# Kernel optimization log

Hardware: AMD Instinct MI355X
Metric: run time of the kernel (lower is better)

The kernel has to match this reference:

```python
import jax, jax.numpy as jnp
import numpy as np

E = 1024      # embed_dim
QH = 16       # query heads
KVH = 4       # kv heads
HD = E // QH  # head_dim = 64
KVE = HD * KVH  # 256
EPS = 1e-5
ROPE_BASE = 10000.0


def rope(x, d):
    # Faithful to the source RoPE: d == number of heads (x.shape[-2]),
    # and the 'sequence' axis of the cache is x.shape[0] (the batch dim).
    # rope(x) = x*cos + (x*sin) * neg_half(x)  (note: nonlinear in x).
    b = x.shape[0]
    theta = 1.0 / (ROPE_BASE ** (jnp.arange(0, d, 2, dtype=jnp.float32) / d))  # (d//2,)
    seq_idx = jnp.arange(b, dtype=jnp.float32)                                 # (b,)
    idx_theta = seq_idx[:, None] * theta[None, :]                              # (b, d//2)
    idx2 = jnp.concatenate([idx_theta, idx_theta], axis=-1)                    # (b, d)
    # cached shape (b,1,1,d); source permutes (0,1,3,2) -> (b,1,d,1)
    cos = jnp.cos(idx2)[:, None, :, None]  # (b,1,d,1)
    sin = jnp.sin(idx2)[:, None, :, None]
    d2 = d // 2
    # split of the LAST dim (head_dim) at d//2 == num_heads//2, as in source
    neg = jnp.concatenate([-x[..., d2:], x[..., :d2]], axis=-1)
    return x * cos + (x * sin) * neg


def setup_inputs() -> dict:
    key = jax.random.key(0)
    ks = jax.random.split(key, 12)
    b, n = 1, 2048

    def xavier(k, shape):
        fan_out, fan_in = shape
        std = (2.0 / (fan_in + fan_out)) ** 0.5
        return jax.random.normal(k, shape, dtype=jnp.float32) * std

    return {
        "query": jax.random.normal(ks[0], (b, n, E), dtype=jnp.float32),
        "key": jax.random.normal(ks[1], (b, n, E), dtype=jnp.float32),
        "value": jax.random.normal(ks[2], (b, n, E), dtype=jnp.float32),
        "Wq": xavier(ks[3], (E, E)),
        "bq": jnp.zeros((E,), jnp.float32),
        "Wk": xavier(ks[4], (KVE, E)),
        "bk": jnp.zeros((KVE,), jnp.float32),
        "Wv": xavier(ks[5], (KVE, E)),
        "bv": jnp.zeros((KVE,), jnp.float32),
        "gamma": jnp.ones((E,), jnp.float32),
        "beta": jnp.zeros((E,), jnp.float32),
    }


def reference(query, key, value, Wq, bq, Wk, bk, Wv, bv, gamma, beta):
    b, n, _ = query.shape
    q = query @ Wq.T + bq            # (b,n,E)
    k = key @ Wk.T + bk              # (b,n,KVE)
    v = value @ Wv.T + bv            # (b,n,KVE)

    q = q.reshape(b, n, QH, HD)      # b n h d
    k = k.reshape(b, n, KVH, HD)
    v = v.reshape(b, n, KVH, HD)

    q = rope(q, QH)
    k = rope(k, KVH)

    # b n h d -> b h n d
    q = jnp.transpose(q, (0, 2, 1, 3))
    k = jnp.transpose(k, (0, 2, 1, 3))
    v = jnp.transpose(v, (0, 2, 1, 3))

    scale = float(HD) ** 0.5
    q = q / scale

    g = QH // KVH
    # 'b (h g) n d -> b g h n d' : h outer, g inner
    q = q.reshape(b, KVH, g, n, HD)              # (b, h, g, n, d)
    q = jnp.transpose(q, (0, 2, 1, 3, 4))        # (b, g, h, n, d)

    sim = jnp.einsum('bghnd,bhsd->bghns', q, k)  # (b,g,h,n,s)
    attn = jax.nn.softmax(sim, axis=-1)
    out = jnp.einsum('bghns,bhsd->bghnd', attn, v)

    # 'b g h n d -> b n (h g) d'
    out = jnp.transpose(out, (0, 3, 2, 1, 4))    # (b, n, h, g, d)
    x = out.reshape(b, n, QH * HD)               # (b, n, E)

    # LayerNorm (biased variance, as in torch)
    mu = jnp.mean(x, axis=-1, keepdims=True)
    var = jnp.mean((x - mu) ** 2, axis=-1, keepdims=True)
    x = (x - mu) * jax.lax.rsqrt(var + EPS) * gamma + beta

    # NOTE: source computes out_proj(x) but returns x, so out_proj is dead code.
    return x
```

## Files before the change

### kernel.cpp

```cpp
#include <hip/hip_runtime.h>
#include <math.h>

#define EDIM   1024
#define KVEDIM 256
#define HDIM   64
#define QHEADS 16

typedef __attribute__((ext_vector_type(8))) short short8;
typedef __attribute__((ext_vector_type(4))) float f32x4;

__device__ __forceinline__ unsigned pack2(float a, float b) {
    unsigned ua = __builtin_bit_cast(unsigned, a);
    unsigned ub = __builtin_bit_cast(unsigned, b);
    ua += 0x7fffu + ((ua >> 16) & 1u);
    ub += 0x7fffu + ((ub >> 16) & 1u);
    return (ua >> 16) | (ub & 0xffff0000u);
}
__device__ __forceinline__ short f2b(float a) {
    unsigned ua = __builtin_bit_cast(unsigned, a);
    ua += 0x7fffu + ((ua >> 16) & 1u);
    return (short)(ua >> 16);
}
__device__ __forceinline__ unsigned cvtpk(float a, float b) {
    unsigned r;
    asm("v_cvt_pk_bf16_f32 %0, %1, %2" : "=v"(r) : "v"(a), "v"(b));
    return r;
}

__global__ __launch_bounds__(256)
void cvt_bf16(const float* __restrict__ s0, const float* __restrict__ s1,
              const float* __restrict__ s2, const float* __restrict__ s3,
              const float* __restrict__ s4, const float* __restrict__ s5,
              short* __restrict__ d0, short* __restrict__ d1,
              short* __restrict__ d2, short* __restrict__ d3,
              short* __restrict__ d4, short* __restrict__ d5,
              int n0, int n1, int n2, int n3, int n4, int n5)
{
    const float* s; short* d; int n;
    switch (blockIdx.y) {
        case 0: s = s0; d = d0; n = n0; break;
        case 1: s = s1; d = d1; n = n1; break;
        case 2: s = s2; d = d2; n = n2; break;
        case 3: s = s3; d = d3; n = n3; break;
        case 4: s = s4; d = d4; n = n4; break;
        default: s = s5; d = d5; n = n5; break;
    }
    int i = ((int)blockIdx.x * 256 + threadIdx.x) * 8;
    if (i >= n) return;
    float4 a = *(const float4*)&s[i];
    float4 b = *(const float4*)&s[i + 4];
    uint4 o;
    o.x = pack2(a.x, a.y); o.y = pack2(a.z, a.w);
    o.z = pack2(b.x, b.y); o.w = pack2(b.z, b.w);
    *(uint4*)&d[i] = o;
}

__global__ __launch_bounds__(256)
void proj_gemm(const short* __restrict__ Aq, const short* __restrict__ Ak,
               const short* __restrict__ Av,
               const short* __restrict__ Wqb, const short* __restrict__ Wkb,
               const short* __restrict__ Wvb,
               const float* __restrict__ bq, const float* __restrict__ bk,
               const float* __restrict__ bv,
               short* __restrict__ Cq, short* __restrict__ Ck,
               short* __restrict__ Cv, float qscale)
{
    const int bid = blockIdx.x;
    const short* A; const short* W; const float* bias; short* C;
    int N, bm, bn; float scale;
    if (bid < 128) {
        A = Aq; W = Wqb; bias = bq; C = Cq; N = EDIM; scale = qscale;
        bm = (bid >> 3) * 128; bn = (bid & 7) * 128;
    } else if (bid < 160) {
        int i = bid - 128;
        A = Ak; W = Wkb; bias = bk; C = Ck; N = KVEDIM; scale = 1.0f;
        bm = (i >> 1) * 128; bn = (i & 1) * 128;
    } else {
        int i = bid - 160;
        A = Av; W = Wvb; bias = bv; C = Cv; N = KVEDIM; scale = 1.0f;
        bm = (i >> 1) * 128; bn = (i & 1) * 128;
    }
    const int K = EDIM;

    __shared__ short As[128 * 72];
    __shared__ short Ws[128 * 72];

    const int t = threadIdx.x, lane = t & 63, wv = t >> 6;
    const int lm = lane & 15, quad = lane >> 4;
    const int q8 = quad * 8, q4 = quad * 4;
    const int wm = (wv & 1) * 64, wn = (wv >> 1) * 64;
    const int sr = t >> 3, sc = (t & 7) * 8;

    f32x4 zero = {0.f, 0.f, 0.f, 0.f};
    f32x4 acc[4][4];
    #pragma unroll
    for (int i = 0; i < 4; ++i)
        #pragma unroll
        for (int j = 0; j < 4; ++j) acc[i][j] = zero;

    for (int k0 = 0; k0 < K; k0 += 64) {
        __syncthreads();
        #pragma unroll
        for (int i = 0; i < 4; ++i) {
            int r = sr + i * 32;
            *(uint4*)&As[r * 72 + sc] = *(const uint4*)&A[(size_t)(bm + r) * K + k0 + sc];
            *(uint4*)&Ws[r * 72 + sc] = *(const uint4*)&W[(size_t)(bn + r) * K + k0 + sc];
        }
        __syncthreads();
        #pragma unroll
        for (int ks = 0; ks < 2; ++ks) {
            short8 af[4], bfr[4];
            #pragma unroll
            for (int i = 0; i < 4; ++i)
                af[i] = *(const short8*)&As[(wm + i * 16 + lm) * 72 + ks * 32 + q8];
            #pragma unroll
            for (int j = 0; j < 4; ++j)
                bfr[j] = *(const short8*)&Ws[(wn + j * 16 + lm) * 72 + ks * 32 + q8];
            #pragma unroll
            for (int i = 0; i < 4; ++i)
                #pragma unroll
                for (int j = 0; j < 4; ++j)
                    acc[i][j] = __builtin_amdgcn_mfma_f32_16x16x32_bf16(
                        af[i], bfr[j], acc[i][j], 0, 0, 0);
        }
    }

    #pragma unroll
    for (int j = 0; j < 4; ++j) {
        float bj = bias[bn + wn + j * 16 + lm];
        #pragma unroll
        for (int i = 0; i < 4; ++i)
            #pragma unroll
            for (int r = 0; r < 4; ++r)
                C[(size_t)(bm + wm + i * 16 + q4 + r) * N + bn + wn + j * 16 + lm] =
                    f2b((acc[i][j][r] + bj) * scale);
    }
}

__global__ __launch_bounds__(256)
void attn_mfma(const short* __restrict__ q, const short* __restrict__ k,
               const short* __restrict__ v, float* __restrict__ x,
               float* __restrict__ opart, float* __restrict__ lpart,
               int n, int s_len, int partial)
{
    __shared__ short Ks[64 * 72];
    __shared__ short Vt[64 * 72];
    __shared__ short Ps[64 * 72];
    __shared__ float Lred[4][64];

    const int qh = blockIdx.y, kvh = qh >> 2;
    const int r0 = blockIdx.x * 64;
    const int t = threadIdx.x;
    const int lane = t & 63, wv = t >> 6;
    const int lm = lane & 15, quad = lane >> 4;
    const int q8 = quad * 8, q4 = quad * 4;

    short8 qf[4][2];
    #pragma unroll
    for (int qt = 0; qt < 4; ++qt) {
        const short* qrow = &q[(size_t)(r0 + qt * 16 + lm) * EDIM + qh * HDIM];
        qf[qt][0] = *(const short8*)&qrow[q8];
        qf[qt][1] = *(const short8*)&qrow[32 + q8];
    }

    const int rt0 = (wv & 1) * 2;
    const int dt0 = (wv >> 1) * 2;

    f32x4 zero = {0.f, 0.f, 0.f, 0.f};
    f32x4 oacc[2][2];
    #pragma unroll
    for (int i = 0; i < 2; ++i)
        #pragma unroll
        for (int j = 0; j < 2; ++j) oacc[i][j] = zero;
    float lp[4] = {0.f, 0.f, 0.f, 0.f};

    const int krow = t >> 2, kc = (t & 3) * 8;
    const int vs4 = (t & 15) * 4, vd0 = (t >> 4) * 4;

    const int s_lo = (int)blockIdx.z * s_len;
    for (int s0 = s_lo; s0 < s_lo + s_len; s0 += 64) {
        __syncthreads();
        {
            const uint4* ksrc = (const uint4*)&k[(size_t)(s0 + krow) * KVEDIM + kvh * HDIM];
            uint4 ka = ksrc[t & 3];
            uint4 kb = ksrc[(t & 3) + 4];
            *(uint4*)&Ks[krow * 72 + kc] = ka;
            *(uint4*)&Ks[krow * 72 + kc + 32] = kb;
        }
        {
            unsigned vr[4][2];
            #pragma unroll
            for (int i = 0; i < 4; ++i) {
                uint2 vv = *(const uint2*)&v[(size_t)(s0 + vs4 + i) * KVEDIM + kvh * HDIM + vd0];
                vr[i][0] = vv.x; vr[i][1] = vv.y;
            }
            #pragma unroll
            for (int j = 0; j < 4; ++j) {
                const unsigned sel = (j & 1) ? 0x07060302u : 0x05040100u;
                const int w = j >> 1;
                uint2 o;
                o.x = __builtin_amdgcn_perm(vr[1][w], vr[0][w], sel);
                o.y = __builtin_amdgcn_perm(vr[3][w], vr[2][w], sel);
                *(uint2*)&Vt[(vd0 + j) * 72 + vs4] = o;
            }
        }
        __syncthreads();

        short8 kf0 = *(const short8*)&Ks[(wv * 16 + lm) * 72 + q8];
        short8 kf1 = *(const short8*)&Ks[(wv * 16 + lm) * 72 + 32 + q8];
        #pragma unroll
        for (int qt = 0; qt < 4; ++qt) {
            f32x4 s = zero;
            s = __builtin_amdgcn_mfma_f32_16x16x32_bf16(kf0, qf[qt][0], s, 0, 0, 0);
            s = __builtin_amdgcn_mfma_f32_16x16x32_bf16(kf1, qf[qt][1], s, 0, 0, 0);
            float p0 = exp2f(s[0]);
            float p1 = exp2f(s[1]);
            float p2 = exp2f(s[2]);
            float p3 = exp2f(s[3]);
            lp[qt] += (p0 + p1) + (p2 + p3);
            uint2 pw; pw.x = cvtpk(p0, p1); pw.y = cvtpk(p2, p3);
            *(uint2*)&Ps[(qt * 16 + lm) * 72 + wv * 16 + q4] = pw;
        }
        __syncthreads();

        short8 vf[2][2];
        #pragma unroll
        for (int j = 0; j < 2; ++j) {
            vf[j][0] = *(const short8*)&Vt[((dt0 + j) * 16 + lm) * 72 + q8];
            vf[j][1] = *(const short8*)&Vt[((dt0 + j) * 16 + lm) * 72 + 32 + q8];
        }
        #pragma unroll
        for (int i = 0; i < 2; ++i) {
            short8 pf0 = *(const short8*)&Ps[((rt0 + i) * 16 + lm) * 72 + q8];
            short8 pf1 = *(const short8*)&Ps[((rt0 + i) * 16 + lm) * 72 + 32 + q8];
            #pragma unroll
            for (int j = 0; j < 2; ++j) {
                oacc[i][j] = __builtin_amdgcn_mfma_f32_16x16x32_bf16(pf0, vf[j][0], oacc[i][j], 0, 0, 0);
                oacc[i][j] = __builtin_amdgcn_mfma_f32_16x16x32_bf16(pf1, vf[j][1], oacc[i][j], 0, 0, 0);
            }
        }
    }

    #pragma unroll
    for (int qt = 0; qt < 4; ++qt) {
        float l = lp[qt];
        l += __shfl_xor(l, 16);
        l += __shfl_xor(l, 32);
        if (lane < 16) Lred[wv][qt * 16 + lm] = l;
    }
    __syncthreads();

    if (partial) {
        float* xp = opart + (size_t)blockIdx.z * n * EDIM;
        #pragma unroll
        for (int i = 0; i < 2; ++i) {
            #pragma unroll
            for (int r = 0; r < 4; ++r) {
                int row = (rt0 + i) * 16 + q4 + r;
                float lsum = (Lred[0][row] + Lred[1][row]) + (Lred[2][row] + Lred[3][row]);
                if (dt0 == 0 && lm == 0)
                    lpart[(size_t)blockIdx.z * n * QHEADS + (size_t)(r0 + row) * QHEADS + qh] = lsum;
                #pragma unroll
                for (int j = 0; j < 2; ++j)
                    xp[(size_t)(r0 + row) * EDIM + qh * HDIM + (dt0 + j) * 16 + lm] =
                        oacc[i][j][r];
            }
        }
    } else {
        #pragma unroll
        for (int i = 0; i < 2; ++i) {
            #pragma unroll
            for (int r = 0; r < 4; ++r) {
                int row = (rt0 + i) * 16 + q4 + r;
                float lsum = (Lred[0][row] + Lred[1][row]) + (Lred[2][row] + Lred[3][row]);
                float inv = 1.0f / lsum;
                #pragma unroll
                for (int j = 0; j < 2; ++j)
                    x[(size_t)(r0 + row) * EDIM + qh * HDIM + (dt0 + j) * 16 + lm] =
                        oacc[i][j][r] * inv;
            }
        }
    }
}

__global__ __launch_bounds__(256)
void ln_kernel(float* __restrict__ x, const float* __restrict__ gamma,
               const float* __restrict__ beta,
               const float* __restrict__ opart, const float* __restrict__ lpart,
               int nsplit, int n)
{
    const int row = blockIdx.x;
    const int t = threadIdx.x;

    float4 xv;
    if (nsplit > 0) {
        const int head = t >> 4;
        float l = 0.f;
        float4 s = {0.f, 0.f, 0.f, 0.f};
        for (int z = 0; z < nsplit; ++z) {
            const float4 o = *(const float4*)&opart[(size_t)z * n * EDIM +
                                                    (size_t)row * EDIM + t * 4];
            s.x += o.x; s.y += o.y; s.z += o.z; s.w += o.w;
            l += lpart[(size_t)z * n * QHEADS + (size_t)row * QHEADS + head];
        }
        const float inv = 1.f / l;
        xv.x = s.x * inv; xv.y = s.y * inv; xv.z = s.z * inv; xv.w = s.w * inv;
    } else {
        xv = *(const float4*)&x[(size_t)row * EDIM + t * 4];
    }

    float sm  = xv.x + xv.y + xv.z + xv.w;
    float sq = xv.x * xv.x + xv.y * xv.y + xv.z * xv.z + xv.w * xv.w;
    #pragma unroll
    for (int m = 1; m < 64; m <<= 1) {
        sm += __shfl_xor(sm, m);
        sq += __shfl_xor(sq, m);
    }
    __shared__ float ws_[4], wq_[4];
    const int wave = t >> 6;
    if ((t & 63) == 0) { ws_[wave] = sm; wq_[wave] = sq; }
    __syncthreads();
    sm = ws_[0] + ws_[1] + ws_[2] + ws_[3];
    sq = wq_[0] + wq_[1] + wq_[2] + wq_[3];

    const float mu   = sm * (1.f / EDIM);
    const float var  = sq * (1.f / EDIM) - mu * mu;
    const float rstd = rsqrtf(var + 1e-5f);

    float4 g = *(const float4*)&gamma[t * 4];
    float4 b = *(const float4*)&beta[t * 4];
    float4 o;
    o.x = (xv.x - mu) * rstd * g.x + b.x;
    o.y = (xv.y - mu) * rstd * g.y + b.y;
    o.z = (xv.z - mu) * rstd * g.z + b.z;
    o.w = (xv.w - mu) * rstd * g.w + b.w;
    *(float4*)&x[(size_t)row * EDIM + t * 4] = o;
}

extern "C" void kernel_launch(void* const* d_in, const int* in_sizes, int n_in,
                              void* d_out, int out_size, void* d_ws, size_t ws_size,
                              hipStream_t stream)
{
    const float* query = (const float*)d_in[0];
    const float* key   = (const float*)d_in[1];
    const float* value = (const float*)d_in[2];
    const float* Wq    = (const float*)d_in[3];
    const float* bq    = (const float*)d_in[4];
    const float* Wk    = (const float*)d_in[5];
    const float* bk    = (const float*)d_in[6];
    const float* Wv    = (const float*)d_in[7];
    const float* bv    = (const float*)d_in[8];
    const float* gamma = (const float*)d_in[9];
    const float* beta  = (const float*)d_in[10];
    float* out = (float*)d_out;

    const int n = in_sizes[0] / EDIM;

    short* qa  = (short*)d_ws;
    short* ka  = qa  + (size_t)n * EDIM;
    short* va  = ka  + (size_t)n * EDIM;
    short* wqb = va  + (size_t)n * EDIM;
    short* wkb = wqb + (size_t)EDIM * EDIM;
    short* wvb = wkb + (size_t)KVEDIM * EDIM;
    short* qb  = wvb + (size_t)KVEDIM * EDIM;
    short* kb  = qb  + (size_t)n * EDIM;
    short* vb  = kb  + (size_t)n * KVEDIM;
    short* ws_end = vb + (size_t)n * KVEDIM;

    const size_t base_bytes = (size_t)((char*)ws_end - (char*)d_ws);
    int nsplit = 0;
    for (int cand = 4; cand >= 1; cand >>= 1) {
        if (n % (64 * cand)) continue;
        size_t need = base_bytes +
                      (size_t)cand * ((size_t)n * EDIM + (size_t)n * QHEADS) * sizeof(float);
        if (need <= ws_size) { nsplit = cand; break; }
    }
    float* opart = (float*)ws_end;
    float* lpart = opart + (size_t)(nsplit > 0 ? nsplit : 1) * n * EDIM;

    const float qscale = 0.125f * 1.44269504088896f;

    cvt_bf16<<<dim3(1024, 6), 256, 0, stream>>>(
        query, key, value, Wq, Wk, Wv,
        qa, ka, va, wqb, wkb, wvb,
        n * EDIM, n * EDIM, n * EDIM, EDIM * EDIM, KVEDIM * EDIM, KVEDIM * EDIM);

    proj_gemm<<<dim3(192), 256, 0, stream>>>(
        qa, ka, va, wqb, wkb, wvb, bq, bk, bv, qb, kb, vb, qscale);

    const int zdim  = (nsplit > 0) ? nsplit : 1;
    const int s_len = n / zdim;
    attn_mfma<<<dim3(n / 64, QHEADS, zdim), 256, 0, stream>>>(
        qb, kb, vb, out, opart, lpart, n, s_len, nsplit > 0 ? 1 : 0);

    ln_kernel<<<dim3(n), 256, 0, stream>>>(out, gamma, beta, opart, lpart, nsplit, n);
}
```

Measured before the change: 173.4 us.

## Restructure attention: one block per KV head, four query heads share K/V tiles

The attention kernel now assigns each block 16 query rows for one KV head, with each of the four waves handling one grouped query head. K/V tiles are loaded once per block and shared across the GQA group. Probabilities stay in registers as MFMA A-operands instead of passing through shared memory, which removes the P buffer and one barrier per tile. K/V loads are register-prefetched for the next tile, LDS uses XOR swizzling instead of padding, and the split-K factor is fixed at 2 with occupancy hint 4. The risk is smaller per-block work and more blocks, with each block still issuing a full K/V stream.

Measured after the change: 162.4 us. 6.3% less time.

```diff
diff --git a/kernel.cpp b/kernel.cpp
--- a/kernel.cpp
+++ b/kernel.cpp
@@ -137,148 +137,145 @@
     }
 }
 
-__global__ __launch_bounds__(256)
+__global__ __launch_bounds__(256, 4)
 void attn_mfma(const short* __restrict__ q, const short* __restrict__ k,
                const short* __restrict__ v, float* __restrict__ x,
                float* __restrict__ opart, float* __restrict__ lpart,
                int n, int s_len, int partial)
 {
-    __shared__ short Ks[64 * 72];
-    __shared__ short Vt[64 * 72];
-    __shared__ short Ps[64 * 72];
-    __shared__ float Lred[4][64];
-
-    const int qh = blockIdx.y, kvh = qh >> 2;
-    const int r0 = blockIdx.x * 64;
-    const int t = threadIdx.x;
-    const int lane = t & 63, wv = t >> 6;
-    const int lm = lane & 15, quad = lane >> 4;
-    const int q8 = quad * 8, q4 = quad * 4;
-
-    short8 qf[4][2];
-    #pragma unroll
-    for (int qt = 0; qt < 4; ++qt) {
-        const short* qrow = &q[(size_t)(r0 + qt * 16 + lm) * EDIM + qh * HDIM];
-        qf[qt][0] = *(const short8*)&qrow[q8];
-        qf[qt][1] = *(const short8*)&qrow[32 + q8];
-    }
-
-    const int rt0 = (wv & 1) * 2;
-    const int dt0 = (wv >> 1) * 2;
-
-    f32x4 zero = {0.f, 0.f, 0.f, 0.f};
-    f32x4 oacc[2][2];
-    #pragma unroll
-    for (int i = 0; i < 2; ++i)
-        #pragma unroll
-        for (int j = 0; j < 2; ++j) oacc[i][j] = zero;
-    float lp[4] = {0.f, 0.f, 0.f, 0.f};
-
-    const int krow = t >> 2, kc = (t & 3) * 8;
-    const int vs4 = (t & 15) * 4, vd0 = (t >> 4) * 4;
+    __shared__ short Ks[64 * 64];
+    __shared__ short Vs[4096];
+
+    const int kvh = blockIdx.y;
+    const int r0  = blockIdx.x * 16;
+    const int t = threadIdx.x, lane = t & 63, wv = t >> 6;
+    const int qh = (kvh << 2) | wv;
+    const int lm = lane & 15, quad = lane >> 4, q8 = quad * 8;
+
+    short8 qf0, qf1;
+    {
+        const short* qp = &q[(size_t)(r0 + lm) * EDIM + qh * HDIM];
+        qf0 = *(const short8*)&qp[q8];
+        qf1 = *(const short8*)&qp[32 + q8];
+    }
+
+    const f32x4 zero = {0.f, 0.f, 0.f, 0.f};
+    f32x4 oacc[4] = {zero, zero, zero, zero};
+    float lp = 0.f;
+
+    const int sr  = t >> 2;
+    const int scs = (t & 3) * 16;
+    const int kw0 = sr * 64 + (scs ^ ((sr & 7) << 3));
+    const int kw1 = sr * 64 + ((scs + 8) ^ ((sr & 7) << 3));
+    const int vs4 = (t & 15) * 4;
+    const int vd0 = (t >> 4) * 4;
+    const int vktp = vs4 >> 5, vqd = (vs4 >> 2) & 3, vhf = (vs4 >> 4) & 1;
+
+    const int krx  = q8 ^ ((lm & 7) << 3);
+    const int krx2 = (32 + q8) ^ ((lm & 7) << 3);
 
     const int s_lo = (int)blockIdx.z * s_len;
-    for (int s0 = s_lo; s0 < s_lo + s_len; s0 += 64) {
+    const int s_hi = s_lo + s_len;
+    const size_t kbase = (size_t)kvh * HDIM;
+
+    uint4 kra, krb;
+    uint2 vrr[4];
+    {
+        const uint4* ks = (const uint4*)&k[(size_t)(s_lo + sr) * KVEDIM + kbase + scs];
+        kra = ks[0]; krb = ks[1];
+        #pragma unroll
+        for (int i = 0; i < 4; ++i)
+            vrr[i] = *(const uint2*)&v[(size_t)(s_lo + vs4 + i) * KVEDIM + kbase + vd0];
+    }
+
+    for (int s0 = s_lo; s0 < s_hi; s0 += 64) {
+        *(uint4*)&Ks[kw0] = kra;
+        *(uint4*)&Ks[kw1] = krb;
+        #pragma unroll
+        for (int j = 0; j < 4; ++j) {
+            const unsigned sel = (j & 1) ? 0x07060302u : 0x05040100u;
+            unsigned a0 = (j < 2) ? vrr[0].x : vrr[0].y;
+            unsigned a1 = (j < 2) ? vrr[1].x : vrr[1].y;
+            unsigned a2 = (j < 2) ? vrr[2].x : vrr[2].y;
+            unsigned a3 = (j < 2) ? vrr[3].x : vrr[3].y;
+            uint2 o;
+            o.x = __builtin_amdgcn_perm(a1, a0, sel);
+            o.y = __builtin_amdgcn_perm(a3, a2, sel);
+            const int dd = vd0 + j;
+            int slot = ((dd >> 4) << 7) + (vktp << 6) + (vqd << 4) + (dd & 15);
+            slot ^= (slot >> 4) & 7;
+            *(uint2*)&Vs[slot * 8 + vhf * 4] = o;
+        }
         __syncthreads();
-        {
-            const uint4* ksrc = (const uint4*)&k[(size_t)(s0 + krow) * KVEDIM + kvh * HDIM];
-            uint4 ka = ksrc[t & 3];
-            uint4 kb = ksrc[(t & 3) + 4];
-            *(uint4*)&Ks[krow * 72 + kc] = ka;
-            *(uint4*)&Ks[krow * 72 + kc + 32] = kb;
-        }
-        {
-            unsigned vr[4][2];
-            #pragma unroll
-            for (int i = 0; i < 4; ++i) {
-                uint2 vv = *(const uint2*)&v[(size_t)(s0 + vs4 + i) * KVEDIM + kvh * HDIM + vd0];
-                vr[i][0] = vv.x; vr[i][1] = vv.y;
-            }
-            #pragma unroll
-            for (int j = 0; j < 4; ++j) {
-                const unsigned sel = (j & 1) ? 0x07060302u : 0x05040100u;
-                const int w = j >> 1;
-                uint2 o;
-                o.x = __builtin_amdgcn_perm(vr[1][w], vr[0][w], sel);
-                o.y = __builtin_amdgcn_perm(vr[3][w], vr[2][w], sel);
-                *(uint2*)&Vt[(vd0 + j) * 72 + vs4] = o;
-            }
+
+        if (s0 + 64 < s_hi) {
+            const uint4* ks = (const uint4*)&k[(size_t)(s0 + 64 + sr) * KVEDIM + kbase + scs];
+            kra = ks[0]; krb = ks[1];
+            #pragma unroll
+            for (int i = 0; i < 4; ++i)
+                vrr[i] = *(const uint2*)&v[(size_t)(s0 + 64 + vs4 + i) * KVEDIM + kbase + vd0];
+        }
+
+        uint2 pa[4];
+        #pragma unroll
+        for (int kt = 0; kt < 4; ++kt) {
+            const int krow = (kt * 16 + lm) * 64;
+            short8 kf0 = *(const short8*)&Ks[krow + krx];
+            short8 kf1 = *(const short8*)&Ks[krow + krx2];
+            f32x4 s = zero;
+            s = __builtin_amdgcn_mfma_f32_16x16x32_bf16(kf0, qf0, s, 0, 0, 0);
+            s = __builtin_amdgcn_mfma_f32_16x16x32_bf16(kf1, qf1, s, 0, 0, 0);
+            float p0 = exp2f(s[0]), p1 = exp2f(s[1]);
+            float p2 = exp2f(s[2]), p3 = exp2f(s[3]);
+            lp += (p0 + p1) + (p2 + p3);
+            pa[kt].x = cvtpk(p0, p1);
+            pa[kt].y = cvtpk(p2, p3);
+        }
+
+        uint4 ap0; ap0.x = pa[0].x; ap0.y = pa[0].y; ap0.z = pa[1].x; ap0.w = pa[1].y;
+        uint4 ap1; ap1.x = pa[2].x; ap1.y = pa[2].y; ap1.z = pa[3].x; ap1.w = pa[3].y;
+        #pragma unroll
+        for (int dt = 0; dt < 4; ++dt) {
+            int sb  = (dt << 7) + (quad << 4) + lm;
+            int sx0 = sb ^ ((sb >> 4) & 7);
+            int sb1 = sb + 64;
+            int sx1 = sb1 ^ ((sb1 >> 4) & 7);
+            oacc[dt] = __builtin_amdgcn_mfma_f32_16x16x32_bf16(
+                __builtin_bit_cast(short8, ap0),
+                *(const short8*)&Vs[sx0 * 8], oacc[dt], 0, 0, 0);
+            oacc[dt] = __builtin_amdgcn_mfma_f32_16x16x32_bf16(
+                __builtin_bit_cast(short8, ap1),
+                *(const short8*)&Vs[sx1 * 8], oacc[dt], 0, 0, 0);
         }
         __syncthreads();
-
-        short8 kf0 = *(const short8*)&Ks[(wv * 16 + lm) * 72 + q8];
-        short8 kf1 = *(const short8*)&Ks[(wv * 16 + lm) * 72 + 32 + q8];
-        #pragma unroll
-        for (int qt = 0; qt < 4; ++qt) {
-            f32x4 s = zero;
-            s = __builtin_amdgcn_mfma_f32_16x16x32_bf16(kf0, qf[qt][0], s, 0, 0, 0);
-            s = __builtin_amdgcn_mfma_f32_16x16x32_bf16(kf1, qf[qt][1], s, 0, 0, 0);
-            float p0 = exp2f(s[0]);
-            float p1 = exp2f(s[1]);
-            float p2 = exp2f(s[2]);
-            float p3 = exp2f(s[3]);
-            lp[qt] += (p0 + p1) + (p2 + p3);
-            uint2 pw; pw.x = cvtpk(p0, p1); pw.y = cvtpk(p2, p3);
-            *(uint2*)&Ps[(qt * 16 + lm) * 72 + wv * 16 + q4] = pw;
-        }
-        __syncthreads();
-
-        short8 vf[2][2];
-        #pragma unroll
-        for (int j = 0; j < 2; ++j) {
-            vf[j][0] = *(const short8*)&Vt[((dt0 + j) * 16 + lm) * 72 + q8];
-            vf[j][1] = *(const short8*)&Vt[((dt0 + j) * 16 + lm) * 72 + 32 + q8];
-        }
-        #pragma unroll
-        for (int i = 0; i < 2; ++i) {
-            short8 pf0 = *(const short8*)&Ps[((rt0 + i) * 16 + lm) * 72 + q8];
-            short8 pf1 = *(const short8*)&Ps[((rt0 + i) * 16 + lm) * 72 + 32 + q8];
-            #pragma unroll
-            for (int j = 0; j < 2; ++j) {
-                oacc[i][j] = __builtin_amdgcn_mfma_f32_16x16x32_bf16(pf0, vf[j][0], oacc[i][j], 0, 0, 0);
-                oacc[i][j] = __builtin_amdgcn_mfma_f32_16x16x32_bf16(pf1, vf[j][1], oacc[i][j], 0, 0, 0);
-            }
-        }
-    }
-
-    #pragma unroll
-    for (int qt = 0; qt < 4; ++qt) {
-        float l = lp[qt];
-        l += __shfl_xor(l, 16);
-        l += __shfl_xor(l, 32);
-        if (lane < 16) Lred[wv][qt * 16 + lm] = l;
-    }
-    __syncthreads();
+    }
+
+    float lt = lp;
+    lt += __shfl_xor(lt, 16);
+    lt += __shfl_xor(lt, 32);
 
     if (partial) {
         float* xp = opart + (size_t)blockIdx.z * n * EDIM;
-        #pragma unroll
-        for (int i = 0; i < 2; ++i) {
-            #pragma unroll
-            for (int r = 0; r < 4; ++r) {
-                int row = (rt0 + i) * 16 + q4 + r;
-                float lsum = (Lred[0][row] + Lred[1][row]) + (Lred[2][row] + Lred[3][row]);
-                if (dt0 == 0 && lm == 0)
-                    lpart[(size_t)blockIdx.z * n * QHEADS + (size_t)(r0 + row) * QHEADS + qh] = lsum;
-                #pragma unroll
-                for (int j = 0; j < 2; ++j)
-                    xp[(size_t)(r0 + row) * EDIM + qh * HDIM + (dt0 + j) * 16 + lm] =
-                        oacc[i][j][r];
-            }
+        if (lane < 16)
+            lpart[(size_t)blockIdx.z * n * QHEADS + (size_t)(r0 + lane) * QHEADS + qh] = lt;
+        #pragma unroll
+        for (int r = 0; r < 4; ++r) {
+            const int row = r0 + quad * 4 + r;
+            #pragma unroll
+            for (int dt = 0; dt < 4; ++dt)
+                xp[(size_t)row * EDIM + qh * HDIM + dt * 16 + lm] = oacc[dt][r];
         }
     } else {
-        #pragma unroll
-        for (int i = 0; i < 2; ++i) {
-            #pragma unroll
-            for (int r = 0; r < 4; ++r) {
-                int row = (rt0 + i) * 16 + q4 + r;
-                float lsum = (Lred[0][row] + Lred[1][row]) + (Lred[2][row] + Lred[3][row]);
-                float inv = 1.0f / lsum;
-                #pragma unroll
-                for (int j = 0; j < 2; ++j)
-                    x[(size_t)(r0 + row) * EDIM + qh * HDIM + (dt0 + j) * 16 + lm] =
-                        oacc[i][j][r] * inv;
-            }
+        float linv[4];
+        #pragma unroll
+        for (int r = 0; r < 4; ++r)
+            linv[r] = 1.0f / __shfl(lt, quad * 4 + r);
+        #pragma unroll
+        for (int r = 0; r < 4; ++r) {
+            const int row = r0 + quad * 4 + r;
+            #pragma unroll
+            for (int dt = 0; dt < 4; ++dt)
+                x[(size_t)row * EDIM + qh * HDIM + dt * 16 + lm] = oacc[dt][r] * linv[r];
         }
     }
 }
@@ -369,11 +366,11 @@
 
     const size_t base_bytes = (size_t)((char*)ws_end - (char*)d_ws);
     int nsplit = 0;
-    for (int cand = 4; cand >= 1; cand >>= 1) {
-        if (n % (64 * cand)) continue;
+    {
+        const int cand = 2;
         size_t need = base_bytes +
                       (size_t)cand * ((size_t)n * EDIM + (size_t)n * QHEADS) * sizeof(float);
-        if (need <= ws_size) { nsplit = cand; break; }
+        if ((n % (64 * cand)) == 0 && need <= ws_size) nsplit = cand;
     }
     float* opart = (float*)ws_end;
     float* lpart = opart + (size_t)(nsplit > 0 ? nsplit : 1) * n * EDIM;
@@ -390,7 +387,7 @@
 
     const int zdim  = (nsplit > 0) ? nsplit : 1;
     const int s_len = n / zdim;
-    attn_mfma<<<dim3(n / 64, QHEADS, zdim), 256, 0, stream>>>(
+    attn_mfma<<<dim3(n / 16, 4, zdim), 256, 0, stream>>>(
         qb, kb, vb, out, opart, lpart, n, s_len, nsplit > 0 ? 1 : 0);
 
     ln_kernel<<<dim3(n), 256, 0, stream>>>(out, gamma, beta, opart, lpart, nsplit, n);
```
